# Kernel tuning notes

Measured on AMD Instinct MI355X. Metric: run time of the kernel, lower is better.

## Reference

```python
import jax, jax.numpy as jnp
import numpy as np

Tx, Ty, Bn = 48, 48, 64
DW, E, D, A = 512, 512, 1024, 512   # dim_wemb, dim_enc, dim_dec, dim_att
VS, VT = 32000, 32000


def setup_inputs() -> dict:
    key = jax.random.key(0)
    ks = iter(jax.random.split(key, 40))
    def p(shape, s=0.05):
        return jax.random.normal(next(ks), shape, jnp.float32) * s
    inp = {
        "x_data": jax.random.randint(next(ks), (Tx, Bn), 0, VS),
        "x_mask": jnp.ones((Tx, Bn), jnp.float32),
        "y_data": jax.random.randint(next(ks), (Ty, Bn), 0, VT),
        "y_mask": jnp.ones((Ty, Bn), jnp.float32),
        "src_emb": p((VS, DW)),
        "dec_emb": p((VT, DW)),
        # encoder bidirectional LSTM (gate order i,f,g,o; b = b_ih + b_hh)
        "enc_Wih_f": p((4 * E, DW)), "enc_Whh_f": p((4 * E, E)), "enc_b_f": jnp.zeros((4 * E,), jnp.float32),
        "enc_Wih_r": p((4 * E, DW)), "enc_Whh_r": p((4 * E, E)), "enc_b_r": jnp.zeros((4 * E,), jnp.float32),
        "h0_W": p((D, 2 * E)), "h0_b": jnp.zeros((D,), jnp.float32),
        "c0_W": p((D, 2 * E)), "c0_b": jnp.zeros((D,), jnp.float32),
        "att1_W": p((A, 2 * E + DW + D)), "att1_b": jnp.zeros((A,), jnp.float32),
        "att2_W": p((1, A)), "att2_b": jnp.zeros((1,), jnp.float32),
        "cell_Wih": p((4 * D, DW + 2 * E)), "cell_Whh": p((4 * D, D)), "cell_b": jnp.zeros((4 * D,), jnp.float32),
        "read_W": p((2 * DW, 2 * E + D + DW)), "read_b": jnp.zeros((2 * DW,), jnp.float32),
        "out_W": p((VT, DW)), "out_b": jnp.zeros((VT,), jnp.float32),
    }
    return inp


def _lstm(x_seq, Wih, Whh, b, reverse):
    # x_seq: [T, B, in]; returns hidden states [T, B, H] (PyTorch LSTM equations)
    B = x_seq.shape[1]
    H = Whh.shape[1]
    def step(carry, x_t):
        h, c = carry
        z = x_t @ Wih.T + h @ Whh.T + b
        i, f, g, o = jnp.split(z, 4, axis=-1)
        c = jax.nn.sigmoid(f) * c + jax.nn.sigmoid(i) * jnp.tanh(g)
        h = jax.nn.sigmoid(o) * jnp.tanh(c)
        return (h, c), h
    init = (jnp.zeros((B, H), x_seq.dtype), jnp.zeros((B, H), x_seq.dtype))
    _, ys = jax.lax.scan(step, init, x_seq, reverse=reverse)
    return ys


def reference(x_data, x_mask, y_data, y_mask, src_emb, dec_emb,
              enc_Wih_f, enc_Whh_f, enc_b_f, enc_Wih_r, enc_Whh_r, enc_b_r,
              h0_W, h0_b, c0_W, c0_b, att1_W, att1_b, att2_W, att2_b,
              cell_Wih, cell_Whh, cell_b, read_W, read_b, out_W, out_b):
    B = x_data.shape[1]
    # ---- encoder ----
    x_emb = src_emb[x_data] * x_mask[..., None]                       # [Tx,B,DW]
    out_f = _lstm(x_emb, enc_Wih_f, enc_Whh_f, enc_b_f, reverse=False)
    out_r = _lstm(x_emb, enc_Wih_r, enc_Whh_r, enc_b_r, reverse=True)
    ctx = jnp.concatenate([out_f, out_r], axis=-1) * x_mask[..., None]  # [Tx,B,2E]
    # ---- decoder init ----
    ctx_mean = (ctx * x_mask[..., None]).sum(0) / x_mask.sum(0)[:, None]
    ht = jnp.tanh(ctx_mean @ h0_W.T + h0_b)
    ct = jnp.tanh(ctx_mean @ c0_W.T + c0_b)
    # split additive-attention weight: ctx part precomputed once (same math as concat)
    W1c = att1_W[:, : 2 * E]
    W1y = att1_W[:, 2 * E: 2 * E + DW]
    W1h = att1_W[:, 2 * E + DW:]
    att_ctx = jnp.einsum('tbe,ae->tba', ctx, W1c) + att1_b            # [Tx,B,A]
    # teacher forcing: y_prev[0] = 0 (like the zero-initialized yt), then y_data shifted
    y_prev = jnp.concatenate([jnp.zeros((1, B), y_data.dtype), y_data[:-1]], axis=0)

    def step(carry, xs):
        ht, ct = carry
        yp, yt, ym = xs
        y_emb = dec_emb[yp]                                           # [B,DW]
        a1 = jnp.tanh(att_ctx + y_emb @ W1y.T + ht @ W1h.T)           # [Tx,B,A]
        a2 = (a1 @ att2_W.T + att2_b)[..., 0]                         # [Tx,B]
        a2 = a2 - jnp.max(a2)                                         # global max, as in torch.max(att2)
        alpha = jnp.exp(a2) * x_mask
        alpha = alpha / (alpha.sum(0, keepdims=True) + 1e-15)
        ctx_t = (alpha[..., None] * ctx).sum(0)                       # [B,2E]
        dec_in = jnp.concatenate([y_emb, ctx_t], axis=1)
        z = dec_in @ cell_Wih.T + ht @ cell_Whh.T + cell_b
        i, f, g, o = jnp.split(z, 4, axis=-1)
        ct = jax.nn.sigmoid(f) * ct + jax.nn.sigmoid(i) * jnp.tanh(g)
        ht = jax.nn.sigmoid(o) * jnp.tanh(ct)
        readin = jnp.concatenate([ctx_t, ht, y_emb], axis=1)
        r = (readin @ read_W.T + read_b).reshape(B, DW, 2).max(-1)    # maxout pairs
        logp = jax.nn.log_softmax(r @ out_W.T + out_b, axis=-1)       # [B,VT]
        nll = -jnp.take_along_axis(logp, yt[:, None], axis=1)[:, 0]
        loss_t = (nll * ym).sum() / B
        return (ht, ct), loss_t

    _, losses = jax.lax.scan(step, (ht, ct), (y_prev, y_data, y_mask))
    return losses.sum()
```

## Files before the change

### kernel.cpp

```cpp
#include <hip/hip_runtime.h>
#include <hip/hip_bf16.h>
#include <math.h>

typedef __attribute__((ext_vector_type(8))) short bf16x8;
typedef __attribute__((ext_vector_type(4))) short bf16x4;
typedef __attribute__((ext_vector_type(4))) float f32x4;
typedef unsigned short u16;
typedef unsigned int u32;

__device__ __forceinline__ float bf2f(u16 u) {
    union { float f; u32 i; } v; v.i = ((u32)u) << 16; return v.f;
}
__device__ __forceinline__ float bflo(u32 v) {
    union { float f; u32 u; } x; x.u = v << 16; return x.f;
}
__device__ __forceinline__ float bfhi(u32 v) {
    union { float f; u32 u; } x; x.u = v & 0xFFFF0000u; return x.f;
}
__device__ __forceinline__ u16 f2bf(float x) {
    union { float f; u32 u; } v; v.f = x;
    u32 r = v.u + 0x7FFF + ((v.u >> 16) & 1);
    return (u16)(r >> 16);
}
__device__ __forceinline__ u32 f2bf2(float a, float b) {
    return (u32)f2bf(a) | ((u32)f2bf(b) << 16);
}
__device__ __forceinline__ float sigf(float x) { return 1.0f / (1.0f + expf(-x)); }

__device__ __forceinline__ void st_wt_u16(u16* p, u16 v) {
    asm volatile("global_store_short %0, %1, off sc0 sc1" :: "v"(p), "v"((u32)v) : "memory");
}
__device__ __forceinline__ void st_wt_f32(float* p, float v) {
    asm volatile("global_store_dword %0, %1, off sc0 sc1" :: "v"(p), "v"(v) : "memory");
}
__device__ __forceinline__ void st_wt_u32(u32* p, u32 v) {
    asm volatile("global_store_dword %0, %1, off sc0 sc1" :: "v"(p), "v"(v) : "memory");
}

__device__ __forceinline__ void gbarH(u32* flags, u32* go, int myidx, int aggbid,
                                      u32 ph, int nblk, int nrepmask) {
    __syncthreads();
    if ((int)blockIdx.x == aggbid) {
        if (threadIdx.x == 0) st_wt_u32(flags + (size_t)myidx * 16, ph);
        if (threadIdx.x < 64) {
            bool ok = false;
            if (nblk == 256) {
                const u32* p = flags + (size_t)threadIdx.x * 64;
                while (!ok) {
                    u32 a, b, c, d;
                    asm volatile(
                        "global_load_dword %0, %4, off sc0 sc1\n\t"
                        "global_load_dword %1, %5, off sc0 sc1\n\t"
                        "global_load_dword %2, %6, off sc0 sc1\n\t"
                        "global_load_dword %3, %7, off sc0 sc1\n\t"
                        "s_waitcnt vmcnt(0)"
                        : "=&v"(a), "=&v"(b), "=&v"(c), "=&v"(d)
                        : "v"(p), "v"(p + 16), "v"(p + 32), "v"(p + 48)
                        : "memory");
                    ok = __all((a >= ph) && (b >= ph) && (c >= ph) && (d >= ph));
                    if (!ok) __builtin_amdgcn_s_sleep(2);
                }
            } else {
                const u32* p = flags + (size_t)threadIdx.x * 16;
                while (!ok) {
                    u32 a;
                    asm volatile("global_load_dword %0, %1, off sc0 sc1\n\ts_waitcnt vmcnt(0)"
                                 : "=&v"(a) : "v"(p) : "memory");
                    ok = __all(a >= ph);
                    if (!ok) __builtin_amdgcn_s_sleep(2);
                }
            }
            if ((int)threadIdx.x <= nrepmask)
                st_wt_u32(go + (size_t)threadIdx.x * 16, ph);
        }
        __syncthreads();
    } else {
        if (threadIdx.x == 0) {
            st_wt_u32(flags + (size_t)myidx * 16, ph);
            const u32* gp = go + (size_t)(myidx & nrepmask) * 16;
            u32 v;
            do {
                asm volatile("global_load_dword %0, %1, off sc0 sc1\n\ts_waitcnt vmcnt(0)"
                             : "=&v"(v) : "v"(gp) : "memory");
                if (v < ph) __builtin_amdgcn_s_sleep(1);
            } while (v < ph);
        }
        __syncthreads();
    }
}

template<int OUTBF, int ACT, int CIN>
__global__ __launch_bounds__(256) void mgemm(
    const u16* __restrict__ A, int lda,
    const u16* __restrict__ B, int ldb,
    const float* __restrict__ bias,
    const u16* __restrict__ Cin,
    void* __restrict__ Cout,
    int N, int K,
    const u16* A2, const u16* B2, const float* bias2, const u16* Cin2, void* Cout2)
{
    if (blockIdx.z == 1) { A = A2; B = B2; bias = bias2; Cin = Cin2; Cout = Cout2; }
    const int lane = threadIdx.x & 63;
    const int wave = threadIdx.x >> 6;
    const int wm = wave >> 1, wn = wave & 1;
    const int lr = lane & 15, lg = lane >> 4;
    const size_t bm = (size_t)blockIdx.y * 64, bn = (size_t)blockIdx.x * 64;
    const u16* Ap = A + (bm + wm * 32 + lr) * (size_t)lda + lg * 8;
    const u16* Bp = B + (bn + wn * 32 + lr) * (size_t)ldb + lg * 8;
    f32x4 acc[2][2] = {};
    for (int k0 = 0; k0 < K; k0 += 32) {
        bf16x8 a0 = *(const bf16x8*)(Ap + k0);
        bf16x8 a1 = *(const bf16x8*)(Ap + k0 + 16 * (size_t)lda);
        bf16x8 b0 = *(const bf16x8*)(Bp + k0);
        bf16x8 b1 = *(const bf16x8*)(Bp + k0 + 16 * (size_t)ldb);
        acc[0][0] = __builtin_amdgcn_mfma_f32_16x16x32_bf16(a0, b0, acc[0][0], 0, 0, 0);
        acc[0][1] = __builtin_amdgcn_mfma_f32_16x16x32_bf16(a0, b1, acc[0][1], 0, 0, 0);
        acc[1][0] = __builtin_amdgcn_mfma_f32_16x16x32_bf16(a1, b0, acc[1][0], 0, 0, 0);
        acc[1][1] = __builtin_amdgcn_mfma_f32_16x16x32_bf16(a1, b1, acc[1][1], 0, 0, 0);
    }
    #pragma unroll
    for (int fi = 0; fi < 2; ++fi)
    #pragma unroll
    for (int fj = 0; fj < 2; ++fj) {
        size_t col = bn + wn * 32 + fj * 16 + lr;
        float bv = bias ? bias[col] : 0.0f;
        #pragma unroll
        for (int r = 0; r < 4; ++r) {
            size_t row = bm + wm * 32 + fi * 16 + lg * 4 + r;
            float v = acc[fi][fj][r] + bv;
            if constexpr (CIN) v += bf2f(Cin[row * (size_t)N + col]);
            if constexpr (ACT) v = tanhf(v);
            if constexpr (OUTBF) ((u16*)Cout)[row * (size_t)N + col] = f2bf(v);
            else                 ((float*)Cout)[row * (size_t)N + col] = v;
        }
    }
}

__global__ __launch_bounds__(256, 1) void enc_persist(
    const u16* __restrict__ WhhFg, const u16* __restrict__ WhhRg,
    const u16* __restrict__ preAF, const u16* __restrict__ preAR,
    const float* __restrict__ bF, const float* __restrict__ bR,
    const float* __restrict__ xm,
    u16* hAbuf, u16* hBbuf,
    u16* __restrict__ ctxB, u32* encSync)
{
    const int tid = threadIdx.x, bid = blockIdx.x;
    const int lane = tid & 63, wave = tid >> 6;
    const int lr = lane & 15, lg = lane >> 4;
    const int dir = bid >> 6;
    const int nb = bid & 63;
    const u16* Whh = dir ? WhhRg : WhhFg;
    const u16* preA = dir ? preAR : preAF;
    const float* bias = dir ? bR : bF;
    u16* hbase = dir ? hBbuf : hAbuf;
    u32* flags = encSync + (size_t)dir * 1280;
    u32* go = flags + 1024;
    const int aggbid = dir * 64;
    __shared__ u16 whh[32 * 520];
    __shared__ float zs[64 * 33];
    for (int i = tid; i < 32 * 64; i += 256) {
        int r = i >> 6, c = (i & 63) * 8;
        *(bf16x8*)&whh[r * 520 + c] = *(const bf16x8*)&Whh[(size_t)(nb * 32 + r) * 512 + c];
    }
    __syncthreads();
    const int gb = tid & 63, dl0 = tid >> 6;
    float creg[2] = {0.f, 0.f};
    u32 ph = 0;
    for (int s = 0; s < 48; ++s) {
        const int t = dir ? (47 - s) : s;
        if (s > 0) {
            const u16* hc = hbase + (size_t)s * 32768;
            const u16* Ap = hc + (wave * 16 + lr) * 512 + lg * 8;
            f32x4 acc0 = {}, acc1 = {};
            #pragma unroll 4
            for (int k0 = 0; k0 < 512; k0 += 32) {
                bf16x8 a  = *(const bf16x8*)(Ap + k0);
                bf16x8 b0 = *(const bf16x8*)&whh[lr * 520 + k0 + lg * 8];
                bf16x8 b1 = *(const bf16x8*)&whh[(16 + lr) * 520 + k0 + lg * 8];
                acc0 = __builtin_amdgcn_mfma_f32_16x16x32_bf16(a, b0, acc0, 0, 0, 0);
                acc1 = __builtin_amdgcn_mfma_f32_16x16x32_bf16(a, b1, acc1, 0, 0, 0);
            }
            #pragma unroll
            for (int r = 0; r < 4; ++r) {
                int row = wave * 16 + lg * 4 + r;
                zs[row * 33 + lr] = acc0[r];
                zs[row * 33 + 16 + lr] = acc1[r];
            }
            __syncthreads();
        }
        u16* hnx = hbase + (size_t)(s + 1) * 32768;
        #pragma unroll
        for (int q = 0; q < 2; ++q) {
            int dl = dl0 + q * 4;
            int dg = nb * 8 + dl;
            bf16x4 pa = *(const bf16x4*)&preA[((size_t)t * 64 + gb) * 2048 + nb * 32 + 4 * dl];
            float iv = bf2f((u16)pa[0]) + bias[dg];
            float fv = bf2f((u16)pa[1]) + bias[512 + dg];
            float gv = bf2f((u16)pa[2]) + bias[1024 + dg];
            float ov = bf2f((u16)pa[3]) + bias[1536 + dg];
            if (s > 0) {
                iv += zs[gb * 33 + 4 * dl + 0];
                fv += zs[gb * 33 + 4 * dl + 1];
                gv += zs[gb * 33 + 4 * dl + 2];
                ov += zs[gb * 33 + 4 * dl + 3];
            }
            float cn = sigf(fv) * creg[q] + sigf(iv) * tanhf(gv);
            float hn = sigf(ov) * tanhf(cn);
            creg[q] = cn;
            st_wt_u16(&hnx[gb * 512 + dg], f2bf(hn));
            ctxB[((size_t)t * 64 + gb) * 1024 + dir * 512 + dg] = f2bf(hn * xm[t * 64 + gb]);
        }
        if (s < 47) gbarH(flags, go, nb, aggbid, ++ph, 64, 15);
    }
}

__global__ __launch_bounds__(512, 1) void dec_persist(
    const u16* __restrict__ WzB, const u16* __restrict__ W1hB,
    const u16* __restrict__ attctxB, const u16* __restrict__ ctxB,
    const u16* __restrict__ preYB, const u16* __restrict__ yembB,
    const float* __restrict__ att2W, const float* __restrict__ att2b,
    const float* __restrict__ xmask, const float* __restrict__ cellb,
    u16* htR, const float* __restrict__ ctF,
    float* svB, float* alphaB, const u16* __restrict__ G,
    u16* c3r, u32* decFlags, u32* decGo)
{
    const int tid = threadIdx.x, bid = blockIdx.x;
    const int lane = tid & 63, wave = tid >> 6;
    const int lr = lane & 15, lg = lane >> 4;
    const int cb = ((bid & 7) << 5) | (bid >> 3);
    __shared__ u16 wzl[16 * 1544];
    __shared__ u16 w1h[2 * 1024];
    __shared__ u16 big[48 * 512];
    __shared__ float alds[48 * 64];
    __shared__ float zp[64][17];
    __shared__ float zred[8 * 64 * 17];
    __shared__ float a2s[64];

    for (int i = tid; i < 16 * 192; i += 512) {
        int r = i / 192, c = (i % 192) * 8;
        *(bf16x8*)&wzl[r * 1544 + c] =
            *(const bf16x8*)&WzB[(size_t)(cb * 16 + r) * 2560 + 1024 + c];
    }
    for (int i = tid; i < 256; i += 512) {
        int r = i >> 7, c = (i & 127) * 8;
        *(bf16x8*)&w1h[r * 1024 + c] = *(const bf16x8*)&W1hB[(size_t)(bid * 2 + r) * 1024 + c];
    }
    const int isatt = (bid < 128);
    const int ab = bid >> 1;
    const int eh = bid & 1;
    u32 ctxr[48];
    float a2wreg[8];
    float xmr = 0.f;
    if (isatt) {
        for (int i = tid; i < 48 * 64; i += 512) {
            int tp = i >> 6, c = (i & 63) * 8;
            *(bf16x8*)&big[tp * 512 + c] =
                *(const bf16x8*)&attctxB[((size_t)tp * 64 + ab) * 512 + c];
        }
        if (tid < 256) {
            #pragma unroll
            for (int tp = 0; tp < 48; ++tp)
                ctxr[tp] = *(const u32*)&ctxB[((size_t)tp * 64 + ab) * 1024 + eh * 512 + 2 * tid];
        }
        #pragma unroll
        for (int k = 0; k < 8; ++k) a2wreg[k] = att2W[k * 64 + lane];
        if (tid < 64) xmr = xmask[tid * 64 + ab];
    }
    const int grp = tid >> 6;
    const int zgb = tid & 63;
    uint4 gfrag[12];
    #pragma unroll
    for (int u = 0; u < 6; ++u) {
        const u16* gr = G + ((size_t)(grp * 6 + u) * 64 + zgb) * 4096 + cb * 16;
        gfrag[2 * u]     = *(const uint4*)(gr);
        gfrag[2 * u + 1] = *(const uint4*)(gr + 8);
    }
    __syncthreads();

    const float att2b0 = att2b[0];
    const int gb = tid & 63, gdd = (tid >> 6) & 3;
    const int gd = cb * 4 + gdd;
    float cb_reg[4];
    float ct_reg = 0.f;
    if (tid < 256) {
        #pragma unroll
        for (int g = 0; g < 4; ++g) cb_reg[g] = cellb[g * 1024 + gd];
        ct_reg = ctF[gb * 1024 + gd];
    }

    auto svz_phase = [&](int tt) {
        const u16* htT = htR + (size_t)tt * 65536;
        if (wave < 4) {
            const int jl = wave & 1;
            const int bh = wave >> 1;
            const int j = bid * 2 + jl;
            float* svT = svB + (size_t)tt * 32768;
            bf16x8 wv0 = *(const bf16x8*)&w1h[jl * 1024 + lane * 8];
            bf16x8 wv1 = *(const bf16x8*)&w1h[jl * 1024 + 512 + lane * 8];
            float s[32];
            #pragma unroll 8
            for (int bi = 0; bi < 32; ++bi) {
                const u16* hp = htT + (bh * 32 + bi) * 1024 + lane * 8;
                bf16x8 h0 = *(const bf16x8*)(hp);
                bf16x8 h1 = *(const bf16x8*)(hp + 512);
                float a = 0.f;
                #pragma unroll
                for (int u = 0; u < 8; ++u)
                    a += bf2f((u16)h0[u]) * bf2f((u16)wv0[u])
                       + bf2f((u16)h1[u]) * bf2f((u16)wv1[u]);
                s[bi] = a;
            }
            float* zone = zred + wave * 2080;
            #pragma unroll 8
            for (int bi = 0; bi < 32; ++bi) zone[bi * 65 + lane] = s[bi];
            if (lane < 32) {
                const float* zr = zone + lane * 65;
                float tsum = 0.f;
                #pragma unroll
                for (int q = 0; q < 64; ++q) tsum += zr[q];
                int b = bh * 32 + lane;
                st_wt_f32(&svT[b * 512 + j],
                          tsum + bf2f(preYB[((size_t)tt * 64 + b) * 512 + j]));
            }
        } else {
            const int q = wave - 4;
            const u16* Ah = htT + (q * 16 + lr) * 1024 + lg * 8;
            const u16* Ay = yembB + ((size_t)tt * 64 + q * 16 + lr) * 512 + lg * 8;
            const u16* Bp = &wzl[lr * 1544 + lg * 8];
            f32x4 acc = {};
            #pragma unroll 4
            for (int k0 = 0; k0 < 1024; k0 += 32) {
                bf16x8 a = *(const bf16x8*)(Ah + k0);
                bf16x8 b = *(const bf16x8*)(Bp + k0);
                acc = __builtin_amdgcn_mfma_f32_16x16x32_bf16(a, b, acc, 0, 0, 0);
            }
            #pragma unroll 4
            for (int k0 = 0; k0 < 512; k0 += 32) {
                bf16x8 a = *(const bf16x8*)(Ay + k0);
                bf16x8 b = *(const bf16x8*)(Bp + 1024 + k0);
                acc = __builtin_amdgcn_mfma_f32_16x16x32_bf16(a, b, acc, 0, 0, 0);
            }
            #pragma unroll
            for (int r = 0; r < 4; ++r)
                zp[q * 16 + lg * 4 + r][lr] = acc[r];
        }
    };

    u32 ph = 0;
    svz_phase(0);
    gbarH(decFlags, decGo, bid, 255, ++ph, 256, 31);

    for (int t = 0; t < 48; ++t) {
        if (isatt) {
            const float* svT = svB + (size_t)t * 32768;
            float svr[8];
            #pragma unroll
            for (int k = 0; k < 8; ++k) svr[k] = svT[ab * 512 + k * 64 + lane];
            for (int tp = wave; tp < 48; tp += 8) {
                float s = 0.f;
                #pragma unroll
                for (int k = 0; k < 8; ++k)
                    s += a2wreg[k] * tanhf(bf2f(big[tp * 512 + k * 64 + lane]) + svr[k]);
                #pragma unroll
                for (int m = 32; m; m >>= 1) s += __shfl_xor(s, m);
                if (lane == 0) a2s[tp] = s + att2b0;
            }
            __syncthreads();
            if (tid < 64) {
                float v = (tid < 48) ? a2s[tid] : -1e30f;
                float m = v;
                #pragma unroll
                for (int sh = 32; sh; sh >>= 1) m = fmaxf(m, __shfl_xor(m, sh));
                float e = (tid < 48) ? expf(v - m) * xmr : 0.f;
                float ssum = e;
                #pragma unroll
                for (int sh = 32; sh; sh >>= 1) ssum += __shfl_xor(ssum, sh);
                if (tid < 48) a2s[tid] = e / (ssum + 1e-15f);
            }
            __syncthreads();
            u16* c3rt = c3r + (size_t)t * 64 * 2560;
            if (tid < 256) {
                float c0 = 0.f, c1 = 0.f;
                #pragma unroll
                for (int tp = 0; tp < 48; ++tp) {
                    float al = a2s[tp]; u32 cv = ctxr[tp];
                    c0 += al * bflo(cv); c1 += al * bfhi(cv);
                }
                *(u32*)&c3rt[ab * 2560 + eh * 512 + 2 * tid] = f2bf2(c0, c1);
            } else if (tid < 384) {
                int i = tid - 256;
                *(u32*)&c3rt[ab * 2560 + 2048 + eh * 256 + 2 * i] =
                    *(const u32*)&yembB[((size_t)t * 64 + ab) * 512 + eh * 256 + 2 * i];
            }
            if (eh == 0 && tid < 48)
                st_wt_f32(&alphaB[(size_t)t * 3072 + tid * 64 + ab], a2s[tid]);
        }
        gbarH(decFlags, decGo, bid, 255, ++ph, 256, 31);
        {
            const float* alT = alphaB + (size_t)t * 3072;
            for (int i = tid; i < 3072; i += 512) alds[i] = alT[i];
            __syncthreads();
            {
                float pz[16] = {};
                #pragma unroll
                for (int u = 0; u < 6; ++u) {
                    float al = alds[(grp * 6 + u) * 64 + zgb];
                    uint4 g0 = gfrag[2 * u];
                    uint4 g1 = gfrag[2 * u + 1];
                    pz[0]  += al * bflo(g0.x); pz[1]  += al * bfhi(g0.x);
                    pz[2]  += al * bflo(g0.y); pz[3]  += al * bfhi(g0.y);
                    pz[4]  += al * bflo(g0.z); pz[5]  += al * bfhi(g0.z);
                    pz[6]  += al * bflo(g0.w); pz[7]  += al * bfhi(g0.w);
                    pz[8]  += al * bflo(g1.x); pz[9]  += al * bfhi(g1.x);
                    pz[10] += al * bflo(g1.y); pz[11] += al * bfhi(g1.y);
                    pz[12] += al * bflo(g1.z); pz[13] += al * bfhi(g1.z);
                    pz[14] += al * bflo(g1.w); pz[15] += al * bfhi(g1.w);
                }
                float* zr = &zred[(grp * 64 + zgb) * 17];
                #pragma unroll
                for (int c = 0; c < 16; ++c) zr[c] = pz[c];
            }
            __syncthreads();
            if (tid < 256) {
                float zv[4];
                #pragma unroll
                for (int g = 0; g < 4; ++g) {
                    int c = 4 * gdd + g;
                    float s = cb_reg[g] + zp[gb][c];
                    #pragma unroll
                    for (int grp2 = 0; grp2 < 8; ++grp2)
                        s += zred[(grp2 * 64 + gb) * 17 + c];
                    zv[g] = s;
                }
                float cn = sigf(zv[1]) * ct_reg + sigf(zv[0]) * tanhf(zv[2]);
                float hn = sigf(zv[3]) * tanhf(cn);
                ct_reg = cn;
                u16 hb = f2bf(hn);
                st_wt_u16(&htR[(size_t)(t + 1) * 65536 + gb * 1024 + gd], hb);
                c3r[(size_t)t * 64 * 2560 + gb * 2560 + 1024 + gd] = hb;
            }
        }
        if (t < 47) {
            gbarH(decFlags, decGo, bid, 255, ++ph, 256, 31);
            svz_phase(t + 1);
            gbarH(decFlags, decGo, bid, 255, ++ph, 256, 31);
        }
    }
}

__global__ __launch_bounds__(256) void logits_lsm(
    const u16* __restrict__ A, const u16* __restrict__ B,
    const float* __restrict__ outb, const int* __restrict__ ydata,
    float2* __restrict__ part, float* __restrict__ logy)
{
    const int lane = threadIdx.x & 63;
    const int wave = threadIdx.x >> 6;
    const int wm = wave >> 1, wn = wave & 1;
    const int lr = lane & 15, lg = lane >> 4;
    const size_t bm = (size_t)blockIdx.x * 64, bn = (size_t)blockIdx.y * 64;
    const u16* Ap = A + (bm + wm * 32 + lr) * 512 + lg * 8;
    const u16* Bp = B + (bn + wn * 32 + lr) * 512 + lg * 8;
    f32x4 acc[2][2] = {};
    for (int k0 = 0; k0 < 512; k0 += 32) {
        bf16x8 a0 = *(const bf16x8*)(Ap + k0);
        bf16x8 a1 = *(const bf16x8*)(Ap + k0 + 16 * 512);
        bf16x8 b0 = *(const bf16x8*)(Bp + k0);
        bf16x8 b1 = *(const bf16x8*)(Bp + k0 + 16 * 512);
        acc[0][0] = __builtin_amdgcn_mfma_f32_16x16x32_bf16(a0, b0, acc[0][0], 0, 0, 0);
        acc[0][1] = __builtin_amdgcn_mfma_f32_16x16x32_bf16(a0, b1, acc[0][1], 0, 0, 0);
        acc[1][0] = __builtin_amdgcn_mfma_f32_16x16x32_bf16(a1, b0, acc[1][0], 0, 0, 0);
        acc[1][1] = __builtin_amdgcn_mfma_f32_16x16x32_bf16(a1, b1, acc[1][1], 0, 0, 0);
    }
    __shared__ float sm[64][2];
    __shared__ float ss[64][2];
    const float b0 = outb[bn + wn * 32 + lr];
    const float b1 = outb[bn + wn * 32 + 16 + lr];
    #pragma unroll
    for (int fi = 0; fi < 2; ++fi) {
        #pragma unroll
        for (int r = 0; r < 4; ++r) {
            int rloc = wm * 32 + fi * 16 + lg * 4 + r;
            size_t row = bm + rloc;
            float v0 = acc[fi][0][r] + b0;
            float v1 = acc[fi][1][r] + b1;
            int yt = ydata[row];
            if (yt == (int)(bn + wn * 32 + lr))      logy[row] = v0;
            if (yt == (int)(bn + wn * 32 + 16 + lr)) logy[row] = v1;
            float m = fmaxf(v0, v1);
            #pragma unroll
            for (int sh = 1; sh < 16; sh <<= 1) m = fmaxf(m, __shfl_xor(m, sh));
            float s = expf(v0 - m) + expf(v1 - m);
            #pragma unroll
            for (int sh = 1; sh < 16; sh <<= 1) s += __shfl_xor(s, sh);
            if (lr == 0) { sm[rloc][wn] = m; ss[rloc][wn] = s; }
        }
    }
    __syncthreads();
    if (threadIdx.x < 64) {
        float m0 = sm[threadIdx.x][0], m1 = sm[threadIdx.x][1];
        float m = fmaxf(m0, m1);
        float s = ss[threadIdx.x][0] * expf(m0 - m) + ss[threadIdx.x][1] * expf(m1 - m);
        part[(bm + threadIdx.x) * 500 + blockIdx.y] = make_float2(m, s);
    }
}

__global__ __launch_bounds__(64) void lsm_reduce(
    const float2* __restrict__ part, const float* __restrict__ logy,
    const float* __restrict__ ymask, float* __restrict__ lossb)
{
    int r = blockIdx.x, lane = threadIdx.x;
    float m = -1e30f;
    for (int i = lane; i < 500; i += 64) m = fmaxf(m, part[(size_t)r * 500 + i].x);
    #pragma unroll
    for (int sh = 32; sh; sh >>= 1) m = fmaxf(m, __shfl_xor(m, sh));
    float s = 0.f;
    for (int i = lane; i < 500; i += 64) {
        float2 p = part[(size_t)r * 500 + i];
        s += p.y * expf(p.x - m);
    }
    #pragma unroll
    for (int sh = 32; sh; sh >>= 1) s += __shfl_xor(s, sh);
    if (lane == 0) {
        float lp = logy[r] - m - logf(s);
        lossb[r] = -lp * ymask[r] * (1.0f / 64.0f);
    }
}

__global__ void convb(const float* __restrict__ src, int sld, int K,
                      u16* __restrict__ dst, int total)
{
    int idx = blockIdx.x * 256 + threadIdx.x;
    if (idx >= total) return;
    int n = idx / K, k = idx - n * K;
    dst[idx] = f2bf(src[(size_t)n * sld + k]);
}

__global__ void conv_gate4(const float* __restrict__ src, u16* __restrict__ dst,
                           int H, int K, int total)
{
    int idx = blockIdx.x * 256 + threadIdx.x;
    if (idx >= total) return;
    int n = idx / K, k = idx - n * K;
    int d = n >> 2, g = n & 3;
    dst[idx] = f2bf(src[(size_t)(g * H + d) * K + k]);
}

__global__ void build_wz_g4(const float* __restrict__ Wih, const float* __restrict__ Whh,
                            u16* __restrict__ Wz)
{
    int idx = blockIdx.x * 256 + threadIdx.x;
    int j = idx % 2560, np = idx / 2560;
    int n = (np & 3) * 1024 + (np >> 2);
    float v;
    if (j < 1024)      v = Wih[(size_t)n * 1536 + 512 + j];
    else if (j < 2048) v = Whh[(size_t)n * 1024 + (j - 1024)];
    else               v = Wih[(size_t)n * 1536 + (j - 2048)];
    Wz[idx] = f2bf(v);
}

__global__ void embed_kernel(const int* __restrict__ xd, const float* __restrict__ xm,
                             const int* __restrict__ yd,
                             const float* __restrict__ src_emb, const float* __restrict__ dec_emb,
                             u16* __restrict__ x_emb, u16* __restrict__ y_emb)
{
    int idx = blockIdx.x * 256 + threadIdx.x;
    int d = idx & 511;
    int tb = idx >> 9;
    if (blockIdx.y == 0) {
        int v = xd[tb];
        x_emb[idx] = f2bf(src_emb[(size_t)v * 512 + d] * xm[tb]);
    } else {
        int t = tb >> 6, b = tb & 63;
        int v = (t == 0) ? 0 : yd[(t - 1) * 64 + b];
        y_emb[idx] = f2bf(dec_emb[(size_t)v * 512 + d]);
    }
}

__global__ __launch_bounds__(256) void ctx_mean_k(const u16* __restrict__ ctxB,
                                                  const float* __restrict__ xm,
                                                  u16* __restrict__ cm)
{
    int b = blockIdx.x, tid = threadIdx.x;
    float msum = 0.f;
    for (int t = 0; t < 48; ++t) msum += xm[t * 64 + b];
    float inv = 1.0f / msum;
    for (int e = tid; e < 1024; e += 256) {
        float s = 0.f;
        for (int t = 0; t < 48; ++t)
            s += bf2f(ctxB[(size_t)(t * 64 + b) * 1024 + e]) * xm[t * 64 + b];
        cm[b * 1024 + e] = f2bf(s * inv);
    }
}

__global__ void maxpair(const u16* __restrict__ rB, u16* __restrict__ rmax)
{
    int idx = blockIdx.x * 256 + threadIdx.x;
    int row = idx >> 9, d = idx & 511;
    float a = bf2f(rB[(size_t)row * 1024 + 2 * d]);
    float b = bf2f(rB[(size_t)row * 1024 + 2 * d + 1]);
    rmax[idx] = f2bf(fmaxf(a, b));
}

__global__ __launch_bounds__(256) void final_sum(const float* __restrict__ lossb,
                                                 float* __restrict__ out)
{
    __shared__ float red[4];
    int tid = threadIdx.x;
    float s = 0.f;
    for (int i = tid; i < 3072; i += 256) s += lossb[i];
    for (int sh = 32; sh; sh >>= 1) s += __shfl_xor(s, sh);
    if ((tid & 63) == 0) red[tid >> 6] = s;
    __syncthreads();
    if (tid == 0) out[0] = red[0] + red[1] + red[2] + red[3];
}

template<int OUTBF, int ACT, int CIN>
static void mg(hipStream_t st, dim3 grid,
               const u16* A, int lda, const u16* B, int ldb,
               const float* bias, const u16* Cin, void* C, int N, int K,
               const u16* A2 = nullptr, const u16* B2 = nullptr,
               const float* bias2 = nullptr, const u16* Cin2 = nullptr, void* C2 = nullptr)
{
    hipLaunchKernelGGL((mgemm<OUTBF, ACT, CIN>), grid, dim3(256), 0, st,
                       A, lda, B, ldb, bias, Cin, C, N, K, A2, B2, bias2, Cin2, C2);
}

extern "C" void kernel_launch(void* const* d_in, const int* in_sizes, int n_in,
                              void* d_out, int out_size, void* d_ws, size_t ws_size,
                              hipStream_t stream)
{
    const int*   x_data    = (const int*)d_in[0];
    const float* x_mask    = (const float*)d_in[1];
    const int*   y_data    = (const int*)d_in[2];
    const float* y_mask    = (const float*)d_in[3];
    const float* src_emb   = (const float*)d_in[4];
    const float* dec_emb   = (const float*)d_in[5];
    const float* enc_Wih_f = (const float*)d_in[6];
    const float* enc_Whh_f = (const float*)d_in[7];
    const float* enc_b_f   = (const float*)d_in[8];
    const float* enc_Wih_r = (const float*)d_in[9];
    const float* enc_Whh_r = (const float*)d_in[10];
    const float* enc_b_r   = (const float*)d_in[11];
    const float* h0_W      = (const float*)d_in[12];
    const float* h0_b      = (const float*)d_in[13];
    const float* c0_W      = (const float*)d_in[14];
    const float* c0_b      = (const float*)d_in[15];
    const float* att1_W    = (const float*)d_in[16];
    const float* att1_b    = (const float*)d_in[17];
    const float* att2_W    = (const float*)d_in[18];
    const float* att2_b    = (const float*)d_in[19];
    const float* cell_Wih  = (const float*)d_in[20];
    const float* cell_Whh  = (const float*)d_in[21];
    const float* cell_b    = (const float*)d_in[22];
    const float* read_W    = (const float*)d_in[23];
    const float* read_b    = (const float*)d_in[24];
    const float* out_W     = (const float*)d_in[25];
    const float* out_b     = (const float*)d_in[26];
    float* out = (float*)d_out;
    (void)in_sizes; (void)n_in; (void)out_size; (void)ws_size;

    char* base = (char*)d_ws;
    size_t off = 0;
    auto ab = [&](size_t bytes) -> void* {
        void* p = base + off;
        off += (bytes + 255) & ~(size_t)255;
        return p;
    };
    u16* WzB     = (u16*)ab(4096UL * 2560 * 2);
    u16* outWB   = (u16*)ab(32000UL * 512 * 2);
    u16* readWB  = (u16*)ab(1024UL * 2560 * 2);
    u16* WihFg   = (u16*)ab(2048UL * 512 * 2);
    u16* WihRg   = (u16*)ab(2048UL * 512 * 2);
    u16* WhhFg   = (u16*)ab(2048UL * 512 * 2);
    u16* WhhRg   = (u16*)ab(2048UL * 512 * 2);
    u16* h0WB    = (u16*)ab(1024UL * 1024 * 2);
    u16* c0WB    = (u16*)ab(1024UL * 1024 * 2);
    u16* W1cB    = (u16*)ab(512UL * 1024 * 2);
    u16* W1yB    = (u16*)ab(512UL * 512 * 2);
    u16* W1hB    = (u16*)ab(512UL * 1024 * 2);
    u16* xembB   = (u16*)ab(3072UL * 512 * 2);
    u16* yembB   = (u16*)ab(3072UL * 512 * 2);
    u16* preAF   = (u16*)ab(3072UL * 2048 * 2);
    u16* preAR   = (u16*)ab(3072UL * 2048 * 2);
    u16* G       = preAF;
    float2* part = (float2*)preAF;
    u16* rB      = (u16*)((char*)preAF + 12288000);
    u16* rmaxB   = (u16*)((char*)preAF + 12288000 + 6291456);
    u16* ctxB    = (u16*)ab(3072UL * 1024 * 2);
    u16* attctxB = (u16*)ab(3072UL * 512 * 2);
    u16* preYB   = (u16*)ab(3072UL * 512 * 2);
    u16* cmB     = (u16*)ab(64UL * 1024 * 2);
    u16* hAbuf   = (u16*)ab(49UL * 64 * 512 * 2);
    u16* hBbuf   = (u16*)ab(49UL * 64 * 512 * 2);
    u16* htR     = (u16*)ab(49UL * 64 * 1024 * 2);
    float* ctF   = (float*)ab(64UL * 1024 * 4);
    float* svB   = (float*)ab(48UL * 64 * 512 * 4);
    float* alphaB= (float*)ab(48UL * 3072 * 4);
    u16* c3r     = (u16*)ab(3072UL * 2560 * 2);
    float* logy  = (float*)ab(3072UL * 4);
    float* lossb = (float*)ab(3072UL * 4);
    u32* sync    = (u32*)ab(32768);
    u32* decFlags = sync;
    u32* decGo    = sync + 4096;
    u32* encSync  = sync + 4608;

    hipMemsetAsync(sync, 0, 32768, stream);
    hipMemsetAsync(hAbuf, 0, 64UL * 512 * 2, stream);
    hipMemsetAsync(hBbuf, 0, 64UL * 512 * 2, stream);
    hipLaunchKernelGGL(build_wz_g4, dim3(40960), dim3(256), 0, stream, cell_Wih, cell_Whh, WzB);
    auto conv = [&](const float* src, int sld, int K, u16* dst, size_t total) {
        hipLaunchKernelGGL(convb, dim3((unsigned)((total + 255) / 256)), dim3(256), 0, stream,
                           src, sld, K, dst, (int)total);
    };
    auto convg = [&](const float* src, u16* dst, int H, int K) {
        size_t total = (size_t)4 * H * K;
        hipLaunchKernelGGL(conv_gate4, dim3((unsigned)((total + 255) / 256)), dim3(256), 0, stream,
                           src, dst, H, K, (int)total);
    };
    conv(out_W, 512, 512, outWB, 32000UL * 512);
    conv(read_W, 2560, 2560, readWB, 1024UL * 2560);
    convg(enc_Wih_f, WihFg, 512, 512);
    convg(enc_Wih_r, WihRg, 512, 512);
    convg(enc_Whh_f, WhhFg, 512, 512);
    convg(enc_Whh_r, WhhRg, 512, 512);
    conv(h0_W, 1024, 1024, h0WB, 1024UL * 1024);
    conv(c0_W, 1024, 1024, c0WB, 1024UL * 1024);
    conv(att1_W, 2560, 1024, W1cB, 512UL * 1024);
    conv(att1_W + 1024, 2560, 512, W1yB, 512UL * 512);
    conv(att1_W + 1536, 2560, 1024, W1hB, 512UL * 1024);
    hipLaunchKernelGGL(embed_kernel, dim3(6144, 2), dim3(256), 0, stream,
                       x_data, x_mask, y_data, src_emb, dec_emb, xembB, yembB);

    mg<1, 0, 0>(stream, dim3(32, 48, 2), xembB, 512, WihFg, 512, nullptr, nullptr,
                preAF, 2048, 512, xembB, WihRg, nullptr, nullptr, preAR);

    hipLaunchKernelGGL(enc_persist, dim3(128), dim3(256), 0, stream,
                       WhhFg, WhhRg, preAF, preAR, enc_b_f, enc_b_r, x_mask,
                       hAbuf, hBbuf, ctxB, encSync);

    mg<1, 0, 0>(stream, dim3(64, 48, 1), ctxB, 1024, WzB, 2560, nullptr, nullptr,
                G, 4096, 1024);

    hipLaunchKernelGGL(ctx_mean_k, dim3(64), dim3(256), 0, stream, ctxB, x_mask, cmB);
    mg<1, 1, 0>(stream, dim3(16, 1, 1), cmB, 1024, h0WB, 1024, h0_b, nullptr, htR, 1024, 1024);
    mg<0, 1, 0>(stream, dim3(16, 1, 1), cmB, 1024, c0WB, 1024, c0_b, nullptr, ctF, 1024, 1024);
    mg<1, 0, 0>(stream, dim3(8, 48, 1), ctxB, 1024, W1cB, 1024, att1_b, nullptr, attctxB, 512, 1024);
    mg<1, 0, 0>(stream, dim3(8, 48, 1), yembB, 512, W1yB, 512, nullptr, nullptr, preYB, 512, 512);

    hipLaunchKernelGGL(dec_persist, dim3(256), dim3(512), 0, stream,
                       WzB, W1hB, attctxB, ctxB, preYB, yembB, att2_W, att2_b,
                       x_mask, cell_b, htR, ctF, svB, alphaB, G, c3r, decFlags, decGo);

    mg<1, 0, 0>(stream, dim3(16, 48, 1), c3r, 2560, readWB, 2560, read_b, nullptr, rB, 1024, 2560);
    hipLaunchKernelGGL(maxpair, dim3(6144), dim3(256), 0, stream, rB, rmaxB);
    hipLaunchKernelGGL(logits_lsm, dim3(48, 500), dim3(256), 0, stream,
                       rmaxB, outWB, out_b, y_data, part, logy);
    hipLaunchKernelGGL(lsm_reduce, dim3(3072), dim3(64), 0, stream, part, logy, y_mask, lossb);
    hipLaunchKernelGGL(final_sum, dim3(1), dim3(256), 0, stream, lossb, out);
}
```

Baseline: 3.181 ms.

## Fuse LSTM cell update into attention blocks, removing one grid barrier per step

```diff
diff --git a/kernel.cpp b/kernel.cpp
--- a/kernel.cpp
+++ b/kernel.cpp
@@ -221,72 +221,62 @@
     const float* __restrict__ att2W, const float* __restrict__ att2b,
     const float* __restrict__ xmask, const float* __restrict__ cellb,
     u16* htR, const float* __restrict__ ctF,
-    float* svB, float* alphaB, const u16* __restrict__ G,
+    float* svB, float* zpartR, const u16* __restrict__ G,
     u16* c3r, u32* decFlags, u32* decGo)
 {
     const int tid = threadIdx.x, bid = blockIdx.x;
     const int lane = tid & 63, wave = tid >> 6;
     const int lr = lane & 15, lg = lane >> 4;
-    const int cb = ((bid & 7) << 5) | (bid >> 3);
-    __shared__ u16 wzl[16 * 1544];
+    __shared__ u16 wzl[32 * 1544];
     __shared__ u16 w1h[2 * 1024];
-    __shared__ u16 big[48 * 512];
-    __shared__ float alds[48 * 64];
-    __shared__ float zp[64][17];
-    __shared__ float zred[8 * 64 * 17];
+    __shared__ float svzs[4 * 2080];
     __shared__ float a2s[64];
-
-    for (int i = tid; i < 16 * 192; i += 512) {
-        int r = i / 192, c = (i % 192) * 8;
-        *(bf16x8*)&wzl[r * 1544 + c] =
-            *(const bf16x8*)&WzB[(size_t)(cb * 16 + r) * 2560 + 1024 + c];
-    }
+    u16* big = wzl;
+
+    const int isatt = (bid < 128);
+    const int ab = bid >> 1;
+    const int eh = bid & 1;
+    const int u = bid - 128;
+    const int su = ((u & 7) << 4) | (u >> 3);
+    const int scol0 = su * 32;
+
     for (int i = tid; i < 256; i += 512) {
         int r = i >> 7, c = (i & 127) * 8;
         *(bf16x8*)&w1h[r * 1024 + c] = *(const bf16x8*)&W1hB[(size_t)(bid * 2 + r) * 1024 + c];
     }
-    const int isatt = (bid < 128);
-    const int ab = bid >> 1;
-    const int eh = bid & 1;
-    u32 ctxr[48];
-    float a2wreg[8];
-    float xmr = 0.f;
     if (isatt) {
         for (int i = tid; i < 48 * 64; i += 512) {
             int tp = i >> 6, c = (i & 63) * 8;
             *(bf16x8*)&big[tp * 512 + c] =
                 *(const bf16x8*)&attctxB[((size_t)tp * 64 + ab) * 512 + c];
         }
-        if (tid < 256) {
-            #pragma unroll
-            for (int tp = 0; tp < 48; ++tp)
-                ctxr[tp] = *(const u32*)&ctxB[((size_t)tp * 64 + ab) * 1024 + eh * 512 + 2 * tid];
-        }
+    } else {
+        for (int i = tid; i < 32 * 192; i += 512) {
+            int r = i / 192, c = (i % 192) * 8;
+            *(bf16x8*)&wzl[r * 1544 + c] =
+                *(const bf16x8*)&WzB[(size_t)(scol0 + r) * 2560 + 1024 + c];
+        }
+    }
+    float a2wreg[8];
+    float xmr = 0.f;
+    uint2 gfrag[48];
+    float cb_reg[4];
+    float ct_reg = 0.f;
+    const int d = eh * 512 + tid;
+    const int n0 = 4 * d;
+    if (isatt) {
         #pragma unroll
         for (int k = 0; k < 8; ++k) a2wreg[k] = att2W[k * 64 + lane];
         if (tid < 64) xmr = xmask[tid * 64 + ab];
-    }
-    const int grp = tid >> 6;
-    const int zgb = tid & 63;
-    uint4 gfrag[12];
-    #pragma unroll
-    for (int u = 0; u < 6; ++u) {
-        const u16* gr = G + ((size_t)(grp * 6 + u) * 64 + zgb) * 4096 + cb * 16;
-        gfrag[2 * u]     = *(const uint4*)(gr);
-        gfrag[2 * u + 1] = *(const uint4*)(gr + 8);
+        #pragma unroll
+        for (int tp = 0; tp < 48; ++tp)
+            gfrag[tp] = *(const uint2*)&G[((size_t)tp * 64 + ab) * 4096 + n0];
+        #pragma unroll
+        for (int g = 0; g < 4; ++g) cb_reg[g] = cellb[g * 1024 + d];
+        ct_reg = ctF[ab * 1024 + d];
     }
     __syncthreads();
-
     const float att2b0 = att2b[0];
-    const int gb = tid & 63, gdd = (tid >> 6) & 3;
-    const int gd = cb * 4 + gdd;
-    float cb_reg[4];
-    float ct_reg = 0.f;
-    if (tid < 256) {
-        #pragma unroll
-        for (int g = 0; g < 4; ++g) cb_reg[g] = cellb[g * 1024 + gd];
-        ct_reg = ctF[gb * 1024 + gd];
-    }
 
     auto svz_phase = [&](int tt) {
         const u16* htT = htR + (size_t)tt * 65536;
@@ -305,12 +295,12 @@
                 bf16x8 h1 = *(const bf16x8*)(hp + 512);
                 float a = 0.f;
                 #pragma unroll
-                for (int u = 0; u < 8; ++u)
-                    a += bf2f((u16)h0[u]) * bf2f((u16)wv0[u])
-                       + bf2f((u16)h1[u]) * bf2f((u16)wv1[u]);
+                for (int q = 0; q < 8; ++q)
+                    a += bf2f((u16)h0[q]) * bf2f((u16)wv0[q])
+                       + bf2f((u16)h1[q]) * bf2f((u16)wv1[q]);
                 s[bi] = a;
             }
-            float* zone = zred + wave * 2080;
+            float* zone = svzs + wave * 2080;
             #pragma unroll 8
             for (int bi = 0; bi < 32; ++bi) zone[bi * 65 + lane] = s[bi];
             if (lane < 32) {
@@ -322,27 +312,34 @@
                 st_wt_f32(&svT[b * 512 + j],
                           tsum + bf2f(preYB[((size_t)tt * 64 + b) * 512 + j]));
             }
-        } else {
-            const int q = wave - 4;
-            const u16* Ah = htT + (q * 16 + lr) * 1024 + lg * 8;
-            const u16* Ay = yembB + ((size_t)tt * 64 + q * 16 + lr) * 512 + lg * 8;
-            const u16* Bp = &wzl[lr * 1544 + lg * 8];
-            f32x4 acc = {};
+        } else if (!isatt) {
+            const int bt = wave - 4;
+            const u16* Ah = htT + (bt * 16 + lr) * 1024 + lg * 8;
+            const u16* Ay = yembB + ((size_t)tt * 64 + bt * 16 + lr) * 512 + lg * 8;
+            f32x4 acc0 = {}, acc1 = {};
             #pragma unroll 4
             for (int k0 = 0; k0 < 1024; k0 += 32) {
                 bf16x8 a = *(const bf16x8*)(Ah + k0);
-                bf16x8 b = *(const bf16x8*)(Bp + k0);
-                acc = __builtin_amdgcn_mfma_f32_16x16x32_bf16(a, b, acc, 0, 0, 0);
+                bf16x8 b0 = *(const bf16x8*)&wzl[lr * 1544 + k0 + lg * 8];
+                bf16x8 b1 = *(const bf16x8*)&wzl[(16 + lr) * 1544 + k0 + lg * 8];
+                acc0 = __builtin_amdgcn_mfma_f32_16x16x32_bf16(a, b0, acc0, 0, 0, 0);
+                acc1 = __builtin_amdgcn_mfma_f32_16x16x32_bf16(a, b1, acc1, 0, 0, 0);
             }
             #pragma unroll 4
             for (int k0 = 0; k0 < 512; k0 += 32) {
                 bf16x8 a = *(const bf16x8*)(Ay + k0);
-                bf16x8 b = *(const bf16x8*)(Bp + 1024 + k0);
-                acc = __builtin_amdgcn_mfma_f32_16x16x32_bf16(a, b, acc, 0, 0, 0);
-            }
+                bf16x8 b0 = *(const bf16x8*)&wzl[lr * 1544 + 1024 + k0 + lg * 8];
+                bf16x8 b1 = *(const bf16x8*)&wzl[(16 + lr) * 1544 + 1024 + k0 + lg * 8];
+                acc0 = __builtin_amdgcn_mfma_f32_16x16x32_bf16(a, b0, acc0, 0, 0, 0);
+                acc1 = __builtin_amdgcn_mfma_f32_16x16x32_bf16(a, b1, acc1, 0, 0, 0);
+            }
+            float* zpT = zpartR + (size_t)tt * 262144;
             #pragma unroll
-            for (int r = 0; r < 4; ++r)
-                zp[q * 16 + lg * 4 + r][lr] = acc[r];
+            for (int r = 0; r < 4; ++r) {
+                int b = bt * 16 + lg * 4 + r;
+                st_wt_f32(&zpT[(size_t)b * 4096 + scol0 + lr], acc0[r]);
+                st_wt_f32(&zpT[(size_t)b * 4096 + scol0 + 16 + lr], acc1[r]);
+            }
         }
     };
 
@@ -378,67 +375,39 @@
                 if (tid < 48) a2s[tid] = e / (ssum + 1e-15f);
             }
             __syncthreads();
-            u16* c3rt = c3r + (size_t)t * 64 * 2560;
+            u16* c3rt = c3r + (size_t)t * 64 * 2560 + (size_t)ab * 2560;
             if (tid < 256) {
                 float c0 = 0.f, c1 = 0.f;
                 #pragma unroll
                 for (int tp = 0; tp < 48; ++tp) {
-                    float al = a2s[tp]; u32 cv = ctxr[tp];
+                    float al = a2s[tp];
+                    u32 cv = *(const u32*)&ctxB[((size_t)tp * 64 + ab) * 1024 + eh * 512 + 2 * tid];
                     c0 += al * bflo(cv); c1 += al * bfhi(cv);
                 }
-                *(u32*)&c3rt[ab * 2560 + eh * 512 + 2 * tid] = f2bf2(c0, c1);
+                *(u32*)&c3rt[eh * 512 + 2 * tid] = f2bf2(c0, c1);
             } else if (tid < 384) {
                 int i = tid - 256;
-                *(u32*)&c3rt[ab * 2560 + 2048 + eh * 256 + 2 * i] =
+                *(u32*)&c3rt[2048 + eh * 256 + 2 * i] =
                     *(const u32*)&yembB[((size_t)t * 64 + ab) * 512 + eh * 256 + 2 * i];
             }
-            if (eh == 0 && tid < 48)
-                st_wt_f32(&alphaB[(size_t)t * 3072 + tid * 64 + ab], a2s[tid]);
-        }
-        gbarH(decFlags, decGo, bid, 255, ++ph, 256, 31);
-        {
-            const float* alT = alphaB + (size_t)t * 3072;
-            for (int i = tid; i < 3072; i += 512) alds[i] = alT[i];
-            __syncthreads();
-            {
-                float pz[16] = {};
-                #pragma unroll
-                for (int u = 0; u < 6; ++u) {
-                    float al = alds[(grp * 6 + u) * 64 + zgb];
-                    uint4 g0 = gfrag[2 * u];
-                    uint4 g1 = gfrag[2 * u + 1];
-                    pz[0]  += al * bflo(g0.x); pz[1]  += al * bfhi(g0.x);
-                    pz[2]  += al * bflo(g0.y); pz[3]  += al * bfhi(g0.y);
-                    pz[4]  += al * bflo(g0.z); pz[5]  += al * bfhi(g0.z);
-                    pz[6]  += al * bflo(g0.w); pz[7]  += al * bfhi(g0.w);
-                    pz[8]  += al * bflo(g1.x); pz[9]  += al * bfhi(g1.x);
-                    pz[10] += al * bflo(g1.y); pz[11] += al * bfhi(g1.y);
-                    pz[12] += al * bflo(g1.z); pz[13] += al * bfhi(g1.z);
-                    pz[14] += al * bflo(g1.w); pz[15] += al * bfhi(g1.w);
-                }
-                float* zr = &zred[(grp * 64 + zgb) * 17];
-                #pragma unroll
-                for (int c = 0; c < 16; ++c) zr[c] = pz[c];
-            }
-            __syncthreads();
-            if (tid < 256) {
-                float zv[4];
-                #pragma unroll
-                for (int g = 0; g < 4; ++g) {
-                    int c = 4 * gdd + g;
-                    float s = cb_reg[g] + zp[gb][c];
-                    #pragma unroll
-                    for (int grp2 = 0; grp2 < 8; ++grp2)
-                        s += zred[(grp2 * 64 + gb) * 17 + c];
-                    zv[g] = s;
-                }
-                float cn = sigf(zv[1]) * ct_reg + sigf(zv[0]) * tanhf(zv[2]);
-                float hn = sigf(zv[3]) * tanhf(cn);
-                ct_reg = cn;
-                u16 hb = f2bf(hn);
-                st_wt_u16(&htR[(size_t)(t + 1) * 65536 + gb * 1024 + gd], hb);
-                c3r[(size_t)t * 64 * 2560 + gb * 2560 + 1024 + gd] = hb;
-            }
+            float4 zp4 = *(const float4*)&zpartR[(size_t)t * 262144 + (size_t)ab * 4096 + n0];
+            float zv0 = cb_reg[0] + zp4.x;
+            float zv1 = cb_reg[1] + zp4.y;
+            float zv2 = cb_reg[2] + zp4.z;
+            float zv3 = cb_reg[3] + zp4.w;
+            #pragma unroll
+            for (int tp = 0; tp < 48; ++tp) {
+                float al = a2s[tp];
+                uint2 g2 = gfrag[tp];
+                zv0 += al * bflo(g2.x); zv1 += al * bfhi(g2.x);
+                zv2 += al * bflo(g2.y); zv3 += al * bfhi(g2.y);
+            }
+            float cn = sigf(zv1) * ct_reg + sigf(zv0) * tanhf(zv2);
+            float hn = sigf(zv3) * tanhf(cn);
+            ct_reg = cn;
+            u16 hb = f2bf(hn);
+            st_wt_u16(&htR[(size_t)(t + 1) * 65536 + ab * 1024 + d], hb);
+            c3rt[1024 + d] = hb;
         }
         if (t < 47) {
             gbarH(decFlags, decGo, bid, 255, ++ph, 256, 31);
@@ -695,7 +664,7 @@
     u16* htR     = (u16*)ab(49UL * 64 * 1024 * 2);
     float* ctF   = (float*)ab(64UL * 1024 * 4);
     float* svB   = (float*)ab(48UL * 64 * 512 * 4);
-    float* alphaB= (float*)ab(48UL * 3072 * 4);
+    float* zpartR= (float*)ab(48UL * 64 * 4096 * 4);
     u16* c3r     = (u16*)ab(3072UL * 2560 * 2);
     float* logy  = (float*)ab(3072UL * 4);
     float* lossb = (float*)ab(3072UL * 4);
@@ -749,7 +718,7 @@
 
     hipLaunchKernelGGL(dec_persist, dim3(256), dim3(512), 0, stream,
                        WzB, W1hB, attctxB, ctxB, preYB, yembB, att2_W, att2_b,
-                       x_mask, cell_b, htR, ctF, svB, alphaB, G, c3r, decFlags, decGo);
+                       x_mask, cell_b, htR, ctF, svB, zpartR, G, c3r, decFlags, decGo);
 
     mg<1, 0, 0>(stream, dim3(16, 48, 1), c3r, 2560, readWB, 2560, read_b, nullptr, rB, 1024, 2560);
     hipLaunchKernelGGL(maxpair, dim3(6144), dim3(256), 0, stream, rB, rmaxB);
```

New measurement: 4.352 ms. 36.8% more time.
